# Kernel optimization log

Measured on AMD Instinct MI355X. Metric: run time of the kernel, lower is better.

The kernel has to match this reference:

```python
import jax, jax.numpy as jnp
import numpy as np

B, T, DIM, H, BUCKET = 4, 4096, 1024, 16, 64
E = DIM // H          # head dim = 64
U = T // BUCKET       # number of buckets = 64
EPS = 1e-6


def setup_inputs() -> dict:
    key = jax.random.key(0)
    ks = jax.random.split(key, 5)
    scale = 1.0 / np.sqrt(DIM)
    return {
        "x": jax.random.normal(ks[0], (B, T, DIM), dtype=jnp.float32),
        "Wq": jax.random.normal(ks[1], (DIM, DIM), dtype=jnp.float32) * scale,
        "Wk": jax.random.normal(ks[2], (DIM, DIM), dtype=jnp.float32) * scale,
        "Wv": jax.random.normal(ks[3], (DIM, DIM), dtype=jnp.float32) * scale,
        "Wo": jax.random.normal(ks[4], (DIM, DIM), dtype=jnp.float32) * scale,
        "bo": jnp.zeros((DIM,), dtype=jnp.float32),
    }


def _causal_linear_attn(q, k, v):
    # q, k, v: [b, h, t, e]; psi(k) = elu(k) + 1; q softmaxed over feature dim
    q = jax.nn.softmax(q, axis=-1)
    k = jax.nn.elu(k) + 1.0
    bucket = lambda x: x.reshape(*x.shape[:-2], U, BUCKET, E)  # [b,h,u,n,e]
    b_q, b_k, b_v = bucket(q), bucket(k), bucket(v)
    # cumulative key sums per bucket: [b,h,u,d]
    b_k_cumsum = jnp.cumsum(b_k.sum(axis=-2), axis=2)
    # per-bucket context then cumulative over buckets: [b,h,u,d,e]
    context = jnp.einsum("bhund,bhune->bhude", b_k, b_v)
    context = jnp.cumsum(context, axis=2)
    context = context / (b_k_cumsum[..., None] + EPS)
    # shift by one bucket (blindspot): bucket u sees context through bucket u-1
    context = jnp.concatenate(
        [jnp.zeros_like(context[:, :, :1]), context[:, :, :-1]], axis=2
    )
    attn = jnp.einsum("bhund,bhude->bhune", b_q, context)
    return attn.reshape(q.shape)  # [b,h,t,e]


def reference(x, Wq, Wk, Wv, Wo, bo):
    b, t, _ = x.shape
    q = x @ Wq
    k = x @ Wk
    v = x @ Wv
    merge = lambda z: z.reshape(b, t, H, E).transpose(0, 2, 1, 3)  # [b,h,t,e]
    attn = _causal_linear_attn(merge(q), merge(k), merge(v))
    out = attn.transpose(0, 2, 1, 3).reshape(b, t, DIM)
    return out @ Wo + bo
```

## Files before the change

### kernel.cpp

```cpp
#include <hip/hip_runtime.h>


#define T_LEN 4096
#define DIMN  1024
#define NHEAD 16
#define NB    4
#define MROWS (NB * T_LEN)

typedef float f32x4 __attribute__((ext_vector_type(4)));
typedef short s16x8 __attribute__((ext_vector_type(8)));
typedef short s16x4 __attribute__((ext_vector_type(4)));
using u16 = unsigned short;

__device__ __forceinline__ u16 f2bf(float f) {
  unsigned int u = __float_as_uint(f);
  u += 0x7fffu + ((u >> 16) & 1u);
  return (u16)(u >> 16);
}
__device__ __forceinline__ float bf2f(u16 h) {
  return __uint_as_float(((unsigned int)h) << 16);
}
__device__ __forceinline__ int swz16k(int off) {
  return off ^ (((off >> 7) & 3) << 4);
}

__global__ __launch_bounds__(256) void cvt_all_kern(const float* __restrict__ x,
                                                    const float* __restrict__ W0,
                                                    const float* __restrict__ W1,
                                                    const float* __restrict__ W2,
                                                    const float* __restrict__ W3,
                                                    u16* __restrict__ WT,
                                                    u16* __restrict__ xb) {
  __shared__ float tile[64][65];
  const int tid = threadIdx.x;
  if (blockIdx.x < 1024) {
    const int blk = blockIdx.x & 255;
    const int sel = blockIdx.x >> 8;
    const float* W = (sel == 0) ? W0 : (sel == 1) ? W1 : (sel == 2) ? W2 : W3;
    u16* dst = WT + (size_t)sel * DIMN * DIMN;
    const int k0 = (blk >> 4) << 6;
    const int n0 = (blk & 15) << 6;
    const int r = tid >> 6;
    const int c = tid & 63;
#pragma unroll
    for (int i = 0; i < 16; ++i) {
      int row = (i << 2) + r;
      tile[row][c] = W[(size_t)(k0 + row) * DIMN + n0 + c];
    }
    __syncthreads();
#pragma unroll
    for (int i = 0; i < 16; ++i) {
      int row = (i << 2) + r;
      dst[(size_t)(n0 + row) * DIMN + k0 + c] = f2bf(tile[c][row]);
    }
  } else {
    size_t i = ((size_t)(blockIdx.x - 1024) * 256 + tid) * 4;
    f32x4 v = *(const f32x4*)(x + i);
    s16x4 o;
    o.x = (short)f2bf(v.x); o.y = (short)f2bf(v.y);
    o.z = (short)f2bf(v.z); o.w = (short)f2bf(v.w);
    *(s16x4*)(xb + i) = o;
  }
}

template <int MODE>
__global__ __launch_bounds__(512, 4) void gemm_t(
    const u16* __restrict__ A, const u16* __restrict__ Bt,
    u16* __restrict__ dq, u16* __restrict__ dk, u16* __restrict__ dv,
    float* __restrict__ dO, const float* __restrict__ bias) {
  constexpr int K = 1024;
  constexpr int BNT = (MODE == 0) ? 12 : 4;
  constexpr int NT = K / 32;
  __shared__ char lds[73728];

  const int tid = threadIdx.x;
  const int l = tid & 63;
  const int w = tid >> 6;
  const int wm = w >> 2;
  const int wn = w & 3;

  const int xcd = (int)blockIdx.x & 7;
  const int idx = (int)blockIdx.x >> 3;
  const int g = idx / (4 * BNT);
  const int r2 = idx % (4 * BNT);
  const int bn = r2 >> 2;
  const int bm = xcd * 16 + g * 4 + (r2 & 3);
  const size_t arow0 = (size_t)bm * 128;
  const size_t brow0 = (size_t)bn * 256;

  int lrow[2], lcol[2];
#pragma unroll
  for (int i = 0; i < 2; ++i) {
    int lg = swz16k(tid * 16 + i * 8192);
    lrow[i] = lg >> 6;
    lcol[i] = (lg & 63) >> 1;
  }

  const int fr = l & 15;
  const int kswz = (((l >> 4) << 4)) ^ ((((fr >> 1) & 3)) << 4);

  auto STAGE = [&](int buf, int matsel, int tt) {
    const int kbase = (tt & (NT - 1)) * 32;
#pragma unroll
    for (int i = 0; i < 2; ++i) {
      if (matsel == 0 && i == 1) break;
      const u16* src = (matsel == 0)
          ? A  + (arow0 + (size_t)lrow[i]) * K + kbase + lcol[i]
          : Bt + (brow0 + (size_t)lrow[i]) * K + kbase + lcol[i];
      char* dst = lds + (buf * 24576 + matsel * 8192 + i * 8192 + tid * 16);
      __builtin_amdgcn_global_load_lds(
          (__attribute__((address_space(1))) const void*)src,
          (__attribute__((address_space(3))) void*)dst, 16, 0, 0);
    }
  };
  auto LDA = [&](int buf, int rowb) -> s16x8 {
    return *(const s16x8*)(lds + buf * 24576 + rowb * 64 + kswz);
  };
  auto LDB = [&](int buf, int rowb) -> s16x8 {
    return *(const s16x8*)(lds + buf * 24576 + 8192 + rowb * 64 + kswz);
  };

  f32x4 acc[4][4];
#pragma unroll
  for (int i = 0; i < 4; ++i)
#pragma unroll
    for (int j = 0; j < 4; ++j) acc[i][j] = {0.f, 0.f, 0.f, 0.f};

  STAGE(0, 0, 0); STAGE(0, 1, 0);
  STAGE(1, 0, 1); STAGE(1, 1, 1);
  asm volatile("s_waitcnt vmcnt(3)" ::: "memory");
  __builtin_amdgcn_sched_barrier(0);
  __builtin_amdgcn_s_barrier();

  const int amb = wm * 64;
  const int bnb = wn * 64;
  s16x8 af[4], bf[4];

  int bufR = 0, bufW = 2;
#pragma unroll 1
  for (int t = 0; t < NT; ++t) {
    STAGE(bufW, 0, t + 2);
    STAGE(bufW, 1, t + 2);
#pragma unroll
    for (int i = 0; i < 4; ++i) af[i] = LDA(bufR, amb + i * 16 + fr);
#pragma unroll
    for (int i = 0; i < 4; ++i) bf[i] = LDB(bufR, bnb + i * 16 + fr);
    __builtin_amdgcn_s_setprio(1);
#pragma unroll
    for (int mi = 0; mi < 4; ++mi)
#pragma unroll
      for (int ni = 0; ni < 4; ++ni)
        acc[mi][ni] = __builtin_amdgcn_mfma_f32_16x16x32_bf16(
            af[mi], bf[ni], acc[mi][ni], 0, 0, 0);
    __builtin_amdgcn_s_setprio(0);
    asm volatile("s_waitcnt vmcnt(3)" ::: "memory");
    __builtin_amdgcn_sched_barrier(0);
    __builtin_amdgcn_s_barrier();
    bufR = (bufR == 2) ? 0 : bufR + 1;
    bufW = (bufW == 2) ? 0 : bufW + 1;
  }

  const int r0 = (l >> 4) << 2;
  const int c0 = l & 15;
  if constexpr (MODE == 0) {
    const int mat = bn >> 2;
    if (mat == 0) {
      u16* dst = dq;
      const size_t colbase = (size_t)(bn & 3) * 256 + (size_t)wn * 64;
#pragma unroll
      for (int mi = 0; mi < 4; ++mi) {
#pragma unroll
        for (int j = 0; j < 4; ++j) {
          float v0 = acc[mi][0][j], v1 = acc[mi][1][j];
          float v2 = acc[mi][2][j], v3 = acc[mi][3][j];
          float m = fmaxf(fmaxf(v0, v1), fmaxf(v2, v3));
#pragma unroll
          for (int off = 1; off < 16; off <<= 1) m = fmaxf(m, __shfl_xor(m, off));
          float e0 = __expf(v0 - m), e1 = __expf(v1 - m);
          float e2 = __expf(v2 - m), e3 = __expf(v3 - m);
          float s = e0 + e1 + e2 + e3;
#pragma unroll
          for (int off = 1; off < 16; off <<= 1) s += __shfl_xor(s, off);
          float inv = 1.f / s;
          const size_t row = arow0 + wm * 64 + mi * 16 + r0 + j;
          u16* p = dst + row * DIMN + colbase + c0;
          p[0]  = f2bf(e0 * inv); p[16] = f2bf(e1 * inv);
          p[32] = f2bf(e2 * inv); p[48] = f2bf(e3 * inv);
        }
      }
    } else {
      u16* dst = (mat == 1) ? dk : dv;
      const int colb = (bn & 3) * 256 + wn * 64;
#pragma unroll
      for (int mi = 0; mi < 4; ++mi) {
        const size_t row = arow0 + wm * 64 + mi * 16 + r0;
        const int bb = (int)(row >> 12);
        const int t = (int)(row & 4095);
#pragma unroll
        for (int ni = 0; ni < 4; ++ni) {
          const int col = colb + ni * 16 + c0;
          const int h = col >> 6, d = col & 63;
          s16x4 o;
#pragma unroll
          for (int j = 0; j < 4; ++j) {
            float v = acc[mi][ni][j];
            float r = (mat == 1) ? (v > 0.f ? v + 1.f : __expf(v)) : v;
            o[j] = (short)f2bf(r);
          }
          *(s16x4*)&dst[((size_t)((bb * 16 + h) * 64 + d)) * 4096 + t] = o;
        }
      }
    }
  } else {
#pragma unroll
    for (int mi = 0; mi < 4; ++mi)
#pragma unroll
      for (int ni = 0; ni < 4; ++ni) {
        const size_t col = brow0 + (size_t)wn * 64 + ni * 16 + c0;
        const float bv = bias[col];
#pragma unroll
        for (int j = 0; j < 4; ++j) {
          const size_t row = arow0 + wm * 64 + mi * 16 + r0 + j;
          dO[row * DIMN + col] = acc[mi][ni][j] + bv;
        }
      }
  }
}

__global__ __launch_bounds__(256) void mid_fused_kern(const u16* __restrict__ kT,
                                                      const u16* __restrict__ vT,
                                                      const u16* __restrict__ qb,
                                                      u16* __restrict__ attn) {
  __shared__ float cprev[16][68];
  const int tid = threadIdx.x;
  const int l = tid & 63;
  const int w = tid >> 6;
  const int fr = l & 15;
  const int lg = l >> 4;

  const int bid = (int)blockIdx.x;
  const int xcd = bid & 7;
  const int slot = bid >> 3;
  const int bh = xcd * 8 + (slot >> 2);
  const int eg = slot & 3;
  const int b = bh >> 4, h = bh & 15;

  const size_t kvbase = (size_t)bh * 64 * 4096;
  const size_t qrow0 = (size_t)b * T_LEN;

  auto LV = [&](int u, int kk) -> s16x8 {
    return *(const s16x8*)&vT[kvbase + (size_t)(eg * 16 + fr) * 4096 +
                              u * 64 + kk * 32 + lg * 8];
  };
  auto LK = [&](int u, int kk) -> s16x8 {
    return *(const s16x8*)&kT[kvbase + (size_t)(w * 16 + fr) * 4096 +
                              u * 64 + kk * 32 + lg * 8];
  };
  auto LQ = [&](int u, int kk) -> s16x8 {
    return *(const s16x8*)&qb[(qrow0 + u * 64 + w * 16 + fr) * DIMN +
                              (size_t)h * 64 + kk * 32 + lg * 8];
  };

  f32x4 cacc = {0.f, 0.f, 0.f, 0.f};
  float ksum = 0.f;

  s16x8 vA0 = LV(0, 0), vA1 = LV(0, 1);
  s16x8 kB0 = LK(0, 0), kB1 = LK(0, 1);
  s16x8 qA0 = LQ(0, 0), qA1 = LQ(0, 1);

#pragma unroll 1
  for (int u = 0; u < 64; ++u) {
    const s16x8 cvA0 = vA0, cvA1 = vA1;
    const s16x8 ckB0 = kB0, ckB1 = kB1;
    const s16x8 cqA0 = qA0, cqA1 = qA1;
    if (u < 63) {
      vA0 = LV(u + 1, 0); vA1 = LV(u + 1, 1);
      kB0 = LK(u + 1, 0); kB1 = LK(u + 1, 1);
      qA0 = LQ(u + 1, 0); qA1 = LQ(u + 1, 1);
    }
    const float inv = 1.f / (ksum + 1e-6f);
#pragma unroll
    for (int j = 0; j < 4; ++j)
      cprev[lg * 4 + j][w * 16 + fr] = cacc[j] * inv;
    __syncthreads();
    s16x8 cB0, cB1;
#pragma unroll
    for (int kk = 0; kk < 2; ++kk) {
      const float* p = &cprev[fr][kk * 32 + lg * 8];
      f32x4 lo = *(const f32x4*)p;
      f32x4 hi = *(const f32x4*)(p + 4);
      s16x8 t;
      t[0] = (short)f2bf(lo.x); t[1] = (short)f2bf(lo.y);
      t[2] = (short)f2bf(lo.z); t[3] = (short)f2bf(lo.w);
      t[4] = (short)f2bf(hi.x); t[5] = (short)f2bf(hi.y);
      t[6] = (short)f2bf(hi.z); t[7] = (short)f2bf(hi.w);
      if (kk == 0) cB0 = t; else cB1 = t;
    }
    f32x4 aacc = {0.f, 0.f, 0.f, 0.f};
    aacc = __builtin_amdgcn_mfma_f32_16x16x32_bf16(cqA0, cB0, aacc, 0, 0, 0);
    aacc = __builtin_amdgcn_mfma_f32_16x16x32_bf16(cqA1, cB1, aacc, 0, 0, 0);
    const size_t arow = qrow0 + (size_t)u * 64 + w * 16 + lg * 4;
#pragma unroll
    for (int j = 0; j < 4; ++j)
      attn[(arow + j) * DIMN + (size_t)h * 64 + eg * 16 + fr] = f2bf(aacc[j]);
    cacc = __builtin_amdgcn_mfma_f32_16x16x32_bf16(cvA0, ckB0, cacc, 0, 0, 0);
    cacc = __builtin_amdgcn_mfma_f32_16x16x32_bf16(cvA1, ckB1, cacc, 0, 0, 0);
    float s = 0.f;
#pragma unroll
    for (int j = 0; j < 8; ++j)
      s += bf2f((u16)ckB0[j]) + bf2f((u16)ckB1[j]);
    s += __shfl_xor(s, 16);
    s += __shfl_xor(s, 32);
    ksum += s;
    __syncthreads();
  }
}

extern "C" void kernel_launch(void* const* d_in, const int* in_sizes, int n_in,
                              void* d_out, int out_size, void* d_ws, size_t ws_size,
                              hipStream_t stream) {
  const float* x  = (const float*)d_in[0];
  const float* Wq = (const float*)d_in[1];
  const float* Wk = (const float*)d_in[2];
  const float* Wv = (const float*)d_in[3];
  const float* Wo = (const float*)d_in[4];
  const float* bo = (const float*)d_in[5];
  float* out = (float*)d_out;

  constexpr size_t SZ_XB = (size_t)MROWS * DIMN * 2;
  constexpr size_t SZ_WT = (size_t)DIMN * DIMN * 2;
  char* ws = (char*)d_ws;
  u16*   xb   = (u16*)(ws);
  u16*   wqT  = (u16*)(ws + SZ_XB);
  u16*   woT  = (u16*)(ws + SZ_XB + 3 * SZ_WT);
  u16*   qb   = (u16*)(ws + SZ_XB + 4 * SZ_WT);
  u16*   kT   = (u16*)(ws + 2 * SZ_XB + 4 * SZ_WT);
  u16*   vT   = (u16*)(ws + 3 * SZ_XB + 4 * SZ_WT);
  u16*   attn = xb;

  cvt_all_kern<<<1024 + MROWS * DIMN / 1024, 256, 0, stream>>>(x, Wq, Wk, Wv, Wo,
                                                               wqT, xb);

  gemm_t<0><<<1536, 512, 0, stream>>>(xb, wqT, qb, kT, vT, nullptr, nullptr);

  mid_fused_kern<<<256, 256, 0, stream>>>(kT, vT, qb, attn);

  gemm_t<1><<<512, 512, 0, stream>>>(attn, woT, nullptr, nullptr, nullptr, out, bo);
}
```

Baseline: 247.6 us.

## Split mid kernel into context and query warp groups; stage transposed K/V stores through LDS

The mid kernel now runs 512 threads: four waves build the running bucket context and write it as bf16 into a double-buffered LDS slot, while four other waves load Q and apply the previous context. This lets context accumulation overlap with the query products and removes the serial store-sync-load path inside one wave set. The GEMM epilogue for K and V now writes its transposed tile into LDS and then issues contiguous 16-byte global stores, replacing scattered 8-byte strided writes. The LDS reuse needs an extra full wait and barrier after the main loop, and the producer/consumer split depends on one __syncthreads per bucket being matched across both wave groups.

```diff
diff --git a/kernel.cpp b/kernel.cpp
--- a/kernel.cpp
+++ b/kernel.cpp
@@ -91,9 +91,9 @@
   int lrow[2], lcol[2];
 #pragma unroll
   for (int i = 0; i < 2; ++i) {
-    int lg = swz16k(tid * 16 + i * 8192);
-    lrow[i] = lg >> 6;
-    lcol[i] = (lg & 63) >> 1;
+    int lg2 = swz16k(tid * 16 + i * 8192);
+    lrow[i] = lg2 >> 6;
+    lcol[i] = (lg2 & 63) >> 1;
   }
 
   const int fr = l & 15;
@@ -160,6 +160,10 @@
     bufW = (bufW == 2) ? 0 : bufW + 1;
   }
 
+  asm volatile("s_waitcnt vmcnt(0) lgkmcnt(0)" ::: "memory");
+  __builtin_amdgcn_sched_barrier(0);
+  __builtin_amdgcn_s_barrier();
+
   const int r0 = (l >> 4) << 2;
   const int c0 = l & 15;
   if constexpr (MODE == 0) {
@@ -190,16 +194,13 @@
       }
     } else {
       u16* dst = (mat == 1) ? dk : dv;
-      const int colb = (bn & 3) * 256 + wn * 64;
+      u16* lt = (u16*)lds;
 #pragma unroll
       for (int mi = 0; mi < 4; ++mi) {
-        const size_t row = arow0 + wm * 64 + mi * 16 + r0;
-        const int bb = (int)(row >> 12);
-        const int t = (int)(row & 4095);
+        const int tl = wm * 64 + mi * 16 + r0;
 #pragma unroll
         for (int ni = 0; ni < 4; ++ni) {
-          const int col = colb + ni * 16 + c0;
-          const int h = col >> 6, d = col & 63;
+          const int cl = wn * 64 + ni * 16 + c0;
           s16x4 o;
 #pragma unroll
           for (int j = 0; j < 4; ++j) {
@@ -207,8 +208,22 @@
             float r = (mat == 1) ? (v > 0.f ? v + 1.f : __expf(v)) : v;
             o[j] = (short)f2bf(r);
           }
-          *(s16x4*)&dst[((size_t)((bb * 16 + h) * 64 + d)) * 4096 + t] = o;
+          *(s16x4*)&lt[cl * 132 + tl] = o;
         }
+      }
+      __builtin_amdgcn_s_barrier();
+      const int colb = (bn & 3) * 256;
+      const int bb = (int)(arow0 >> 12);
+      const int t0 = (int)(arow0 & 4095);
+#pragma unroll
+      for (int i = 0; i < 8; ++i) {
+        const int chunk = i * 512 + tid;
+        const int cl = chunk >> 4;
+        const int toct = (chunk & 15) * 8;
+        s16x8 vv = *(const s16x8*)&lt[cl * 132 + toct];
+        const int col = colb + cl;
+        const int h = col >> 6, d = col & 63;
+        *(s16x8*)&dst[((size_t)((bb * 16 + h) * 64 + d)) * 4096 + t0 + toct] = vv;
       }
     }
   } else {
@@ -227,14 +242,16 @@
   }
 }
 
-__global__ __launch_bounds__(256) void mid_fused_kern(const u16* __restrict__ kT,
+__global__ __launch_bounds__(512) void mid_fused_kern(const u16* __restrict__ kT,
                                                       const u16* __restrict__ vT,
                                                       const u16* __restrict__ qb,
                                                       u16* __restrict__ attn) {
-  __shared__ float cprev[16][68];
+  __shared__ u16 cprev[2][16][72];
   const int tid = threadIdx.x;
   const int l = tid & 63;
   const int w = tid >> 6;
+  const int ws = w & 3;
+  const bool isCtx = w < 4;
   const int fr = l & 15;
   const int lg = l >> 4;
 
@@ -248,71 +265,68 @@
   const size_t kvbase = (size_t)bh * 64 * 4096;
   const size_t qrow0 = (size_t)b * T_LEN;
 
-  auto LV = [&](int u, int kk) -> s16x8 {
-    return *(const s16x8*)&vT[kvbase + (size_t)(eg * 16 + fr) * 4096 +
-                              u * 64 + kk * 32 + lg * 8];
-  };
-  auto LK = [&](int u, int kk) -> s16x8 {
-    return *(const s16x8*)&kT[kvbase + (size_t)(w * 16 + fr) * 4096 +
-                              u * 64 + kk * 32 + lg * 8];
-  };
-  auto LQ = [&](int u, int kk) -> s16x8 {
-    return *(const s16x8*)&qb[(qrow0 + u * 64 + w * 16 + fr) * DIMN +
-                              (size_t)h * 64 + kk * 32 + lg * 8];
-  };
-
-  f32x4 cacc = {0.f, 0.f, 0.f, 0.f};
-  float ksum = 0.f;
-
-  s16x8 vA0 = LV(0, 0), vA1 = LV(0, 1);
-  s16x8 kB0 = LK(0, 0), kB1 = LK(0, 1);
-  s16x8 qA0 = LQ(0, 0), qA1 = LQ(0, 1);
-
+  if (isCtx) {
+#pragma unroll
+    for (int j = 0; j < 4; ++j) cprev[0][lg * 4 + j][ws * 16 + fr] = 0;
+  }
+  __syncthreads();
+
+  if (isCtx) {
+    auto LV = [&](int u, int kk) -> s16x8 {
+      return *(const s16x8*)&vT[kvbase + (size_t)(eg * 16 + fr) * 4096 +
+                                u * 64 + kk * 32 + lg * 8];
+    };
+    auto LK = [&](int u, int kk) -> s16x8 {
+      return *(const s16x8*)&kT[kvbase + (size_t)(ws * 16 + fr) * 4096 +
+                                u * 64 + kk * 32 + lg * 8];
+    };
+    f32x4 cacc = {0.f, 0.f, 0.f, 0.f};
+    float ksum = 0.f;
+    s16x8 vA0 = LV(0, 0), vA1 = LV(0, 1);
+    s16x8 kB0 = LK(0, 0), kB1 = LK(0, 1);
 #pragma unroll 1
-  for (int u = 0; u < 64; ++u) {
-    const s16x8 cvA0 = vA0, cvA1 = vA1;
-    const s16x8 ckB0 = kB0, ckB1 = kB1;
-    const s16x8 cqA0 = qA0, cqA1 = qA1;
-    if (u < 63) {
-      vA0 = LV(u + 1, 0); vA1 = LV(u + 1, 1);
-      kB0 = LK(u + 1, 0); kB1 = LK(u + 1, 1);
-      qA0 = LQ(u + 1, 0); qA1 = LQ(u + 1, 1);
-    }
-    const float inv = 1.f / (ksum + 1e-6f);
-#pragma unroll
-    for (int j = 0; j < 4; ++j)
-      cprev[lg * 4 + j][w * 16 + fr] = cacc[j] * inv;
-    __syncthreads();
-    s16x8 cB0, cB1;
-#pragma unroll
-    for (int kk = 0; kk < 2; ++kk) {
-      const float* p = &cprev[fr][kk * 32 + lg * 8];
-      f32x4 lo = *(const f32x4*)p;
-      f32x4 hi = *(const f32x4*)(p + 4);
-      s16x8 t;
-      t[0] = (short)f2bf(lo.x); t[1] = (short)f2bf(lo.y);
-      t[2] = (short)f2bf(lo.z); t[3] = (short)f2bf(lo.w);
-      t[4] = (short)f2bf(hi.x); t[5] = (short)f2bf(hi.y);
-      t[6] = (short)f2bf(hi.z); t[7] = (short)f2bf(hi.w);
-      if (kk == 0) cB0 = t; else cB1 = t;
-    }
-    f32x4 aacc = {0.f, 0.f, 0.f, 0.f};
-    aacc = __builtin_amdgcn_mfma_f32_16x16x32_bf16(cqA0, cB0, aacc, 0, 0, 0);
-    aacc = __builtin_amdgcn_mfma_f32_16x16x32_bf16(cqA1, cB1, aacc, 0, 0, 0);
-    const size_t arow = qrow0 + (size_t)u * 64 + w * 16 + lg * 4;
-#pragma unroll
-    for (int j = 0; j < 4; ++j)
-      attn[(arow + j) * DIMN + (size_t)h * 64 + eg * 16 + fr] = f2bf(aacc[j]);
-    cacc = __builtin_amdgcn_mfma_f32_16x16x32_bf16(cvA0, ckB0, cacc, 0, 0, 0);
-    cacc = __builtin_amdgcn_mfma_f32_16x16x32_bf16(cvA1, ckB1, cacc, 0, 0, 0);
-    float s = 0.f;
-#pragma unroll
-    for (int j = 0; j < 8; ++j)
-      s += bf2f((u16)ckB0[j]) + bf2f((u16)ckB1[j]);
-    s += __shfl_xor(s, 16);
-    s += __shfl_xor(s, 32);
-    ksum += s;
-    __syncthreads();
+    for (int u = 0; u < 64; ++u) {
+      const s16x8 cvA0 = vA0, cvA1 = vA1, ckB0 = kB0, ckB1 = kB1;
+      if (u < 63) {
+        vA0 = LV(u + 1, 0); vA1 = LV(u + 1, 1);
+        kB0 = LK(u + 1, 0); kB1 = LK(u + 1, 1);
+      }
+      cacc = __builtin_amdgcn_mfma_f32_16x16x32_bf16(cvA0, ckB0, cacc, 0, 0, 0);
+      cacc = __builtin_amdgcn_mfma_f32_16x16x32_bf16(cvA1, ckB1, cacc, 0, 0, 0);
+      float s = 0.f;
+#pragma unroll
+      for (int j = 0; j < 8; ++j)
+        s += bf2f((u16)ckB0[j]) + bf2f((u16)ckB1[j]);
+      s += __shfl_xor(s, 16);
+      s += __shfl_xor(s, 32);
+      ksum += s;
+      const float inv = 1.f / (ksum + 1e-6f);
+      u16* pp = &cprev[(u + 1) & 1][lg * 4][ws * 16 + fr];
+#pragma unroll
+      for (int j = 0; j < 4; ++j) pp[j * 72] = f2bf(cacc[j] * inv);
+      __syncthreads();
+    }
+  } else {
+    auto LQ = [&](int u, int kk) -> s16x8 {
+      return *(const s16x8*)&qb[(qrow0 + u * 64 + ws * 16 + fr) * DIMN +
+                                (size_t)h * 64 + kk * 32 + lg * 8];
+    };
+    s16x8 qA0 = LQ(0, 0), qA1 = LQ(0, 1);
+#pragma unroll 1
+    for (int u = 0; u < 64; ++u) {
+      const s16x8 cqA0 = qA0, cqA1 = qA1;
+      if (u < 63) { qA0 = LQ(u + 1, 0); qA1 = LQ(u + 1, 1); }
+      s16x8 cB0 = *(const s16x8*)&cprev[u & 1][fr][lg * 8];
+      s16x8 cB1 = *(const s16x8*)&cprev[u & 1][fr][32 + lg * 8];
+      f32x4 aacc = {0.f, 0.f, 0.f, 0.f};
+      aacc = __builtin_amdgcn_mfma_f32_16x16x32_bf16(cqA0, cB0, aacc, 0, 0, 0);
+      aacc = __builtin_amdgcn_mfma_f32_16x16x32_bf16(cqA1, cB1, aacc, 0, 0, 0);
+      const size_t arow = qrow0 + (size_t)u * 64 + ws * 16 + lg * 4;
+#pragma unroll
+      for (int j = 0; j < 4; ++j)
+        attn[(arow + j) * DIMN + (size_t)h * 64 + eg * 16 + fr] = f2bf(aacc[j]);
+      __syncthreads();
+    }
   }
 }
 
@@ -343,7 +357,7 @@
 
   gemm_t<0><<<1536, 512, 0, stream>>>(xb, wqT, qb, kT, vT, nullptr, nullptr);
 
-  mid_fused_kern<<<256, 256, 0, stream>>>(kT, vT, qb, attn);
+  mid_fused_kern<<<256, 512, 0, stream>>>(kT, vT, qb, attn);
 
   gemm_t<1><<<512, 512, 0, stream>>>(attn, woT, nullptr, nullptr, nullptr, out, bo);
 }
```

Measured after the change: 246.5 us. No clear change (-0.5%).
